# Optimization experiments

Measured on AMD Instinct MI355X. Metric: run time of the kernel, lower is better.

The kernel has to match this reference:

```python
import jax, jax.numpy as jnp
import numpy as np

DIS_NORM = 6.0 * 512 / 1000.0  # 6 * D(z=0) * Nmesh / Boxsize with D(0)=1


def setup_inputs() -> dict:
    key = jax.random.key(0)
    x = jax.random.normal(key, (2, 4, 128, 128, 128), dtype=jnp.float32)
    return {"x": x}


def _lag2eul(x):
    N, C = x.shape[0], x.shape[1]
    D, H, W = x.shape[2], x.shape[3], x.shape[4]
    P = D * H * W
    Cout = C - 3 if C > 3 else 1

    # rm_dis_mean=True: mean displacement, detached
    dis_mean = jax.lax.stop_gradient(jnp.mean(x[:, :3], axis=(2, 3, 4), keepdims=True))

    pos = (x[:, :3] - dis_mean) * DIS_NORM  # (N,3,D,H,W)
    gd = jnp.arange(D, dtype=x.dtype) + 0.5
    gh = jnp.arange(H, dtype=x.dtype) + 0.5
    gw = jnp.arange(W, dtype=x.dtype) + 0.5
    grid = jnp.stack(jnp.meshgrid(gd, gh, gw, indexing='ij'))  # (3,D,H,W)
    pos = (pos + grid[None]).reshape(N, 3, P)

    if C > 3:
        val = x[:, 3:].reshape(N, Cout, P)
    else:
        val = jnp.ones((N, Cout, P), dtype=x.dtype)

    intpos = jnp.floor(pos).astype(jnp.int32)
    # 8 trilinear neighbors: bit b of n -> offset along dim b
    neighbors = (jnp.arange(8, dtype=jnp.int32)[None, :] >> jnp.arange(3, dtype=jnp.int32)[:, None]) & 1  # (3,8)
    tgt = intpos[:, :, :, None] + neighbors[None, :, None, :]  # (N,3,P,8)

    kernel = jnp.prod(1.0 - jnp.abs(pos[:, :, :, None] - tgt.astype(x.dtype)), axis=1)  # (N,P,8)
    src = val[:, :, :, None] * kernel[:, None, :, :]  # (N,Cout,P,8)

    # periodic=False: mask out-of-bounds deposits
    bounds = jnp.array([D, H, W], dtype=jnp.int32)[None, :, None, None]
    mask = jnp.all((tgt >= 0) & (tgt < bounds), axis=1)  # (N,P,8)
    ind = (tgt[:, 0] * H + tgt[:, 1]) * W + tgt[:, 2]  # (N,P,8)
    ind = jnp.clip(ind, 0, P - 1)
    src = jnp.where(mask[:, None, :, :], src, jnp.zeros((), dtype=x.dtype))

    def scatter_one(ind_n, src_n):
        mesh = jnp.zeros((Cout, P), dtype=src_n.dtype)
        return mesh.at[:, ind_n.reshape(-1)].add(src_n.reshape(Cout, -1))

    mesh = jax.vmap(scatter_one)(ind, src)  # (N,Cout,P)
    return mesh.reshape(N, Cout, D, H, W)


def reference(x):
    return _lag2eul(x)
```

## Files before the change

kernel.cpp:

```cpp
#include <hip/hip_runtime.h>

#define NBATCH 2
#define NDIM   128
#define NP     (128 * 128 * 128)
#define DIS_NORM 3.072f

#define TS   16
#define LO   5
#define HI   6
#define WIN  (TS + LO + HI)
#define WIN2 (WIN * WIN)
#define WINF (WIN * WIN * WIN)
#define TPB  8
#define NTILE (TPB * TPB * TPB)
#define NTHR 512

#define FXSCALE 16777216.0f
#define FXINV   (1.0f / 16777216.0f)

#define QCAP 1280

#define SLAB 19696

#define SUMS_OFF 0
#define SLABS_OFF 1024
#define WS_FLOATS ((size_t)SLABS_OFF + (size_t)NBATCH * NTILE * SLAB)
#define WS_NEEDED_BYTES (WS_FLOATS * sizeof(float))

__device__ __constant__ int BASE27[27] = {
    0,216,792,972,1548,3084,3564,3744,4224,
    4376,4952,6488,6968,8504,12600,13880,14360,15640,
    16040,16220,16700,16852,17332,18612,19012,19164,19564};

__global__ __launch_bounds__(256) void prep_kernel(const float* __restrict__ x,
                                                   float* __restrict__ ws,
                                                   float* __restrict__ out) {
    const int plane = blockIdx.y;
    if (plane < 6) {
        const int n = plane / 3, c = plane % 3;
        const float4* xp = (const float4*)(x + ((size_t)n * 4 + c) * NP);
        float s = 0.0f;
        for (int i = blockIdx.x * 256 + threadIdx.x; i < NP / 4; i += 128 * 256) {
            float4 v = xp[i];
            s += (v.x + v.y) + (v.z + v.w);
        }
        #pragma unroll
        for (int off = 32; off > 0; off >>= 1) s += __shfl_down(s, off, 64);
        __shared__ float wsum[4];
        if ((threadIdx.x & 63) == 0) wsum[threadIdx.x >> 6] = s;
        __syncthreads();
        if (threadIdx.x == 0)
            ws[SUMS_OFF + plane * 128 + blockIdx.x] =
                (wsum[0] + wsum[1]) + (wsum[2] + wsum[3]);
    } else {
        float4* o4 = (float4*)out;
        const float4 z = make_float4(0.f, 0.f, 0.f, 0.f);
        for (int i = blockIdx.x * 256 + threadIdx.x; i < NBATCH * NP / 4; i += 128 * 256)
            o4[i] = z;
    }
}

__device__ __forceinline__ void load_means128(const float* __restrict__ ws, int n,
                                              float& m0, float& m1, float& m2) {
    float s0 = 0.f, s1 = 0.f, s2 = 0.f;
    const float* p0 = ws + SUMS_OFF + (n * 3 + 0) * 128;
    const float* p1 = ws + SUMS_OFF + (n * 3 + 1) * 128;
    const float* p2 = ws + SUMS_OFF + (n * 3 + 2) * 128;
    #pragma unroll 4
    for (int b = 0; b < 128; ++b) { s0 += p0[b]; s1 += p1[b]; s2 += p2[b]; }
    const float inv_np = 1.0f / (float)NP;
    m0 = s0 * inv_np; m1 = s1 * inv_np; m2 = s2 * inv_np;
}

__device__ __forceinline__ void deposit_pair(unsigned long long* __restrict__ winU,
                                             int b, float va, float vb) {
    const int fa = __float2int_rn(va * FXSCALE);
    const int fb = __float2int_rn(vb * FXSCALE);
    const bool odd = (b & 1);
    const long long packed = (((long long)fb) << 32) + (long long)fa;
    const long long hiOnly = ((long long)fa) << 32;
    atomicAdd(&winU[b >> 1], (unsigned long long)(odd ? hiOnly : packed));
    if (odd) atomicAdd(&winU[(b >> 1) + 1], (unsigned long long)(long long)fb);
}

__device__ __forceinline__ void slow_deposit(unsigned long long* __restrict__ winU,
                                             float* __restrict__ sp,
                                             float pd, float ph, float pw, float v,
                                             int od, int oh, int ow) {
    const float fd = floorf(pd), fh = floorf(ph), fw = floorf(pw);
    const int id = (int)fd, ih = (int)fh, iw = (int)fw;
    const float rd = pd - fd, rh = ph - fh, rw = pw - fw;
    const int wd = id - od, wh = ih - oh, ww = iw - ow;
    const float wd2[2] = {1.0f - rd, rd};
    const float wh2[2] = {1.0f - rh, rh};
    const float ww2[2] = {1.0f - rw, rw};
    #pragma unroll
    for (int dd = 0; dd < 2; ++dd) {
        const int td = id + dd, wdc = wd + dd;
        const bool dW = (unsigned)wdc < WIN, dM = (unsigned)td < NDIM;
        if (!dM && !dW) continue;
        #pragma unroll
        for (int hh = 0; hh < 2; ++hh) {
            const int th = ih + hh, whc = wh + hh;
            const bool hW = (unsigned)whc < WIN, hM = (unsigned)th < NDIM;
            const float vdh = v * wd2[dd] * wh2[hh];
            #pragma unroll
            for (int wi = 0; wi < 2; ++wi) {
                const int tw = iw + wi, wwc = ww + wi;
                const bool wW = (unsigned)wwc < WIN, wM = (unsigned)tw < NDIM;
                const float dep = vdh * ww2[wi];
                if (dW && hW && wW) {
                    const int cb = (wdc * WIN + whc) * WIN + wwc;
                    const int fx = __float2int_rn(dep * FXSCALE);
                    const long long cv = (cb & 1)
                        ? (((long long)fx) << 32) : (long long)fx;
                    atomicAdd(&winU[cb >> 1], (unsigned long long)cv);
                } else if (dM && hM && wM) {
                    atomicAdd(sp + ((size_t)td * NDIM + th) * NDIM + tw, dep);
                }
            }
        }
    }
}

__global__ __launch_bounds__(NTHR, 4) void scatter_tile_kernel(
        const float* __restrict__ x, const float* __restrict__ ws,
        float* __restrict__ slabs, float* __restrict__ out) {
    const int blk = blockIdx.x;
    const int n = blk >> 9;
    const int t = blk & (NTILE - 1);
    const int tx = t & 7, ty = (t >> 3) & 7, tz = t >> 6;

    __shared__ ulonglong2 win2[(WINF + 3) / 4 + 1];
    __shared__ int qcount;
    __shared__ unsigned short queue[QCAP];
    unsigned long long* winU = (unsigned long long*)win2;
    {
        float4* z4 = (float4*)win2;
        const float4 z = make_float4(0.f, 0.f, 0.f, 0.f);
        for (int i = threadIdx.x; i < (WINF + 3) / 4 + 1; i += NTHR) z4[i] = z;
        if (threadIdx.x == 0) qcount = 0;
    }
    float m0, m1, m2;
    load_means128(ws, n, m0, m1, m2);
    __syncthreads();

    const int i0 = threadIdx.x * 8;
    const int lw0 = i0 & 15;
    const int lh  = (i0 >> 4) & 15;
    const int ld  = i0 >> 8;
    const int gd = tz * TS + ld, gh = ty * TS + lh, gw0 = tx * TS + lw0;
    const size_t prow = ((size_t)gd * NDIM + gh) * NDIM + gw0;

    const float4* x4 = (const float4*)(x + (size_t)n * 4 * NP);
    const size_t q = prow >> 2;
    const size_t s4 = NP / 4;
    float4 a0 = x4[0 * s4 + q], a1 = x4[0 * s4 + q + 1];
    float4 b0 = x4[1 * s4 + q], b1 = x4[1 * s4 + q + 1];
    float4 c0 = x4[2 * s4 + q], c1 = x4[2 * s4 + q + 1];
    float4 e0 = x4[3 * s4 + q], e1 = x4[3 * s4 + q + 1];
    const float D0[8] = {a0.x, a0.y, a0.z, a0.w, a1.x, a1.y, a1.z, a1.w};
    const float D1[8] = {b0.x, b0.y, b0.z, b0.w, b1.x, b1.y, b1.z, b1.w};
    const float D2[8] = {c0.x, c0.y, c0.z, c0.w, c1.x, c1.y, c1.z, c1.w};
    const float VV[8] = {e0.x, e0.y, e0.z, e0.w, e1.x, e1.y, e1.z, e1.w};

    const int od = tz * TS - LO, oh = ty * TS - LO, ow = tx * TS - LO;
    float* sp = out + (size_t)n * NP;

    #pragma unroll
    for (int k = 0; k < 8; ++k) {
        const float pd = (D0[k] - m0) * DIS_NORM + (float)gd + 0.5f;
        const float ph = (D1[k] - m1) * DIS_NORM + (float)gh + 0.5f;
        const float pw = (D2[k] - m2) * DIS_NORM + (float)(gw0 + k) + 0.5f;
        const float v = VV[k];

        const float fd = floorf(pd), fh = floorf(ph), fw = floorf(pw);
        const int id = (int)fd, ih = (int)fh, iw = (int)fw;
        const float rd = pd - fd, rh = ph - fh, rw = pw - fw;

        const int wd = id - od, wh = ih - oh, ww = iw - ow;
        if ((unsigned)wd <= WIN - 2 && (unsigned)wh <= WIN - 2 &&
            (unsigned)ww <= WIN - 2) {
            const int b00 = (wd * WIN + wh) * WIN + ww;
            const float sd0 = v * (1.0f - rd), sd1 = v * rd;
            const float h0 = 1.0f - rh, h1 = rh;
            const float q0 = 1.0f - rw, q1 = rw;
            deposit_pair(winU, b00,              sd0 * h0 * q0, sd0 * h0 * q1);
            deposit_pair(winU, b00 + WIN,        sd0 * h1 * q0, sd0 * h1 * q1);
            deposit_pair(winU, b00 + WIN2,       sd1 * h0 * q0, sd1 * h0 * q1);
            deposit_pair(winU, b00 + WIN2 + WIN, sd1 * h1 * q0, sd1 * h1 * q1);
        } else {
            const int qi = atomicAdd(&qcount, 1);
            if (qi < QCAP) {
                queue[qi] = (unsigned short)(i0 + k);
            } else {
                slow_deposit(winU, sp, pd, ph, pw, v, od, oh, ow);
            }
        }
    }

    __syncthreads();

    {
        const int nq = min(qcount, QCAP);
        const float* xb = x + (size_t)n * 4 * NP;
        for (int qi = threadIdx.x; qi < nq; qi += NTHR) {
            const int p = queue[qi];
            const int lw = p & 15, lhq = (p >> 4) & 15, ldq = p >> 8;
            const int gdq = tz * TS + ldq, ghq = ty * TS + lhq, gwq = tx * TS + lw;
            const size_t pr = ((size_t)gdq * NDIM + ghq) * NDIM + gwq;
            const float pd = (xb[pr] - m0) * DIS_NORM + (float)gdq + 0.5f;
            const float ph = (xb[(size_t)NP + pr] - m1) * DIS_NORM + (float)ghq + 0.5f;
            const float pw = (xb[2 * (size_t)NP + pr] - m2) * DIS_NORM + (float)gwq + 0.5f;
            const float v = xb[3 * (size_t)NP + pr];
            slow_deposit(winU, sp, pd, ph, pw, v, od, oh, ow);
        }
    }
    __syncthreads();

    {
        const int NU = (WINF + 1) / 2;
        for (int i = threadIdx.x; i < NU; i += NTHR) {
            const unsigned long long u = winU[i];
            const int lo = (int)(unsigned)(u & 0xffffffffull);
            const int hi = (int)(u >> 32) + (lo < 0 ? 1 : 0);
            float2 f;
            f.x = (float)lo * FXINV;
            f.y = (float)hi * FXINV;
            ((float2*)winU)[i] = f;
        }
    }
    __syncthreads();
    const float* winF = (const float*)winU;

    const int EXTY[3] = {6, 16, 5};
    const int nbase = n << 9;
    for (int r = threadIdx.x; r < WIN2; r += NTHR) {
        const int lz = r / WIN;
        const int ly = r - lz * WIN;
        int mz, pz;
        if (lz < LO) { mz = -1; pz = lz; }
        else if (lz < LO + TS) { mz = 0; pz = lz - LO; }
        else { mz = 1; pz = lz - LO - TS; }
        int my, py;
        if (ly < LO) { my = -1; py = ly; }
        else if (ly < LO + TS) { my = 0; py = ly - LO; }
        else { my = 1; py = ly - LO - TS; }
        const int dtz = tz + mz, dty = ty + my;
        if ((unsigned)dtz >= TPB || (unsigned)dty >= TPB) continue;

        const int jz = 1 - mz, jy = 1 - my;
        const int ey = EXTY[jy];
        const int rowoff = pz * ey + py;
        const int pobase = jz * 9 + jy * 3;
        const float* src = winF + r * WIN;
        const int slabRow = nbase + (dtz * 8 + dty) * 8;

        if (tx > 0) {
            float* d = slabs + (size_t)(slabRow + tx - 1) * SLAB
                     + BASE27[pobase + 2] + rowoff * 5;
            #pragma unroll
            for (int k = 0; k < 5; ++k) d[k] = src[k];
        }
        {
            float* d = slabs + (size_t)(slabRow + tx) * SLAB
                     + BASE27[pobase + 1] + rowoff * 16;
            #pragma unroll
            for (int k = 0; k < 4; ++k) {
                float4 v;
                v.x = src[5 + 4 * k]; v.y = src[6 + 4 * k];
                v.z = src[7 + 4 * k]; v.w = src[8 + 4 * k];
                ((float4*)d)[k] = v;
            }
        }
        if (tx < TPB - 1) {
            float* d = slabs + (size_t)(slabRow + tx + 1) * SLAB
                     + BASE27[pobase + 0] + rowoff * 6;
            #pragma unroll
            for (int k = 0; k < 6; ++k) d[k] = src[21 + k];
        }
    }
}

__global__ __launch_bounds__(NTHR) void gather_tile_kernel(const float* __restrict__ slabs,
                                                           float* __restrict__ out) {
    const int blk = blockIdx.x;
    const int n = blk >> 9;
    const int t = blk & (NTILE - 1);
    const int tx = t & 7, ty = (t >> 3) & 7, tz = t >> 6;

    const float* __restrict__ slab = slabs + (size_t)blk * SLAB;
    float* __restrict__ ob = out + (size_t)n * NP;

    for (int i = threadIdx.x; i < TS * TS * TS; i += NTHR) {
        const int x = i & 15, y = (i >> 4) & 15, z = i >> 8;

        int zt2 = 0, zp2 = 0, ze2 = 0; bool z2 = false;
        if (z < 6)        { if (tz > 0)       { zt2 = 0;  zp2 = z;      ze2 = 6; z2 = true; } }
        else if (z >= 11) { if (tz < TPB - 1) { zt2 = 18; zp2 = z - 11; ze2 = 5; z2 = true; } }
        int yt2 = 0, yp2 = 0, ye2 = 0; bool y2 = false;
        if (y < 6)        { if (ty > 0)       { yt2 = 0;  yp2 = y;      ye2 = 6; y2 = true; } }
        else if (y >= 11) { if (ty < TPB - 1) { yt2 = 6;  yp2 = y - 11; ye2 = 5; y2 = true; } }
        int xt2 = 0, xp2 = 0, xe2 = 0; bool x2 = false;
        if (x < 6)        { if (tx > 0)       { xt2 = 0;  xp2 = x;      xe2 = 6; x2 = true; } }
        else if (x >= 11) { if (tx < TPB - 1) { xt2 = 2;  xp2 = x - 11; xe2 = 5; x2 = true; } }

        float s = slab[BASE27[13] + (z * 16 + y) * 16 + x];
        if (x2) s += slab[BASE27[9 + 3 + xt2] + (z * 16 + y) * xe2 + xp2];
        if (y2) {
            s += slab[BASE27[9 + yt2 + 1] + (z * ye2 + yp2) * 16 + x];
            if (x2) s += slab[BASE27[9 + yt2 + xt2] + (z * ye2 + yp2) * xe2 + xp2];
        }
        if (z2) {
            s += slab[BASE27[zt2 + 3 + 1] + (zp2 * 16 + y) * 16 + x];
            if (x2) s += slab[BASE27[zt2 + 3 + xt2] + (zp2 * 16 + y) * xe2 + xp2];
            if (y2) {
                s += slab[BASE27[zt2 + yt2 + 1] + (zp2 * ye2 + yp2) * 16 + x];
                if (x2) s += slab[BASE27[zt2 + yt2 + xt2] + (zp2 * ye2 + yp2) * xe2 + xp2];
            }
        }

        const size_t g = (((size_t)(tz * TS + z) * NDIM) + ty * TS + y) * NDIM
                       + tx * TS + x;
        ob[g] += s;
    }
}

__global__ __launch_bounds__(256) void scatter_direct_kernel(const float* __restrict__ x,
                                                             const float* __restrict__ ws,
                                                             float* __restrict__ out) {
    const int lin = blockIdx.x * 256 + threadIdx.x;
    const int n = lin >> 21;
    const int p = lin & (NP - 1);

    float m0, m1, m2;
    load_means128(ws, n, m0, m1, m2);

    const size_t base = (size_t)n * 4 * NP;
    const float d0 = x[base + 0 * (size_t)NP + p];
    const float d1 = x[base + 1 * (size_t)NP + p];
    const float d2 = x[base + 2 * (size_t)NP + p];
    const float v  = x[base + 3 * (size_t)NP + p];

    const int w = p & 127, h = (p >> 7) & 127, d = p >> 14;
    const float pd = (d0 - m0) * DIS_NORM + (float)d + 0.5f;
    const float ph = (d1 - m1) * DIS_NORM + (float)h + 0.5f;
    const float pw = (d2 - m2) * DIS_NORM + (float)w + 0.5f;
    const float fd = floorf(pd), fh = floorf(ph), fw = floorf(pw);
    const int id = (int)fd, ih = (int)fh, iw = (int)fw;
    const float rd = pd - fd, rh = ph - fh, rw = pw - fw;
    const float wd[2] = {1.0f - rd, rd}, wh[2] = {1.0f - rh, rh}, ww[2] = {1.0f - rw, rw};
    float* o = out + (size_t)n * NP;
    #pragma unroll
    for (int dd = 0; dd < 2; ++dd) {
        const int td = id + dd;
        if ((unsigned)td >= (unsigned)NDIM) continue;
        #pragma unroll
        for (int hh = 0; hh < 2; ++hh) {
            const int th = ih + hh;
            if ((unsigned)th >= (unsigned)NDIM) continue;
            const float vdh = v * wd[dd] * wh[hh];
            const int rowbase = (td * NDIM + th) * NDIM;
            #pragma unroll
            for (int wi = 0; wi < 2; ++wi) {
                const int tw = iw + wi;
                if ((unsigned)tw >= (unsigned)NDIM) continue;
                atomicAdd(o + rowbase + tw, vdh * ww[wi]);
            }
        }
    }
}

extern "C" void kernel_launch(void* const* d_in, const int* in_sizes, int n_in,
                              void* d_out, int out_size, void* d_ws, size_t ws_size,
                              hipStream_t stream) {
    const float* x = (const float*)d_in[0];
    float* out = (float*)d_out;
    float* ws = (float*)d_ws;
    float* slabs = ws + SLABS_OFF;

    dim3 pgrid(128, 7);

    if (ws_size >= WS_NEEDED_BYTES) {
        prep_kernel<<<pgrid, 256, 0, stream>>>(x, ws, out);
        scatter_tile_kernel<<<dim3(NBATCH * NTILE), NTHR, 0, stream>>>(x, ws, slabs, out);
        gather_tile_kernel<<<dim3(NBATCH * NTILE), NTHR, 0, stream>>>(slabs, out);
    } else {
        prep_kernel<<<pgrid, 256, 0, stream>>>(x, ws, out);
        scatter_direct_kernel<<<dim3(NBATCH * NP / 256), 256, 0, stream>>>(x, ws, out);
    }
}
```

Before: 198.6 us.

## Shrink tile halo, use fixed-point global spill atomics, compute means per block

After: 236.8 us. 19.2% more time.

```diff
diff --git a/kernel.cpp b/kernel.cpp
--- a/kernel.cpp
+++ b/kernel.cpp
@@ -6,8 +6,8 @@
 #define DIS_NORM 3.072f
 
 #define TS   16
-#define LO   5
-#define HI   6
+#define LO   3
+#define HI   4
 #define WIN  (TS + LO + HI)
 #define WIN2 (WIN * WIN)
 #define WINF (WIN * WIN * WIN)
@@ -18,9 +18,9 @@
 #define FXSCALE 16777216.0f
 #define FXINV   (1.0f / 16777216.0f)
 
-#define QCAP 1280
-
-#define SLAB 19696
+#define QCAP 1024
+
+#define SLAB 12168
 
 #define SUMS_OFF 0
 #define SLABS_OFF 1024
@@ -28,9 +28,9 @@
 #define WS_NEEDED_BYTES (WS_FLOATS * sizeof(float))
 
 __device__ __constant__ int BASE27[27] = {
-    0,216,792,972,1548,3084,3564,3744,4224,
-    4376,4952,6488,6968,8504,12600,13880,14360,15640,
-    16040,16220,16700,16852,17332,18612,19012,19164,19564};
+    0,64,320,368,624,1648,1840,1888,2080,
+    2116,2372,3396,3588,4612,8708,9476,9668,10436,
+    10580,10628,10820,10856,11048,11816,11960,11996,12140};
 
 __global__ __launch_bounds__(256) void prep_kernel(const float* __restrict__ x,
                                                    float* __restrict__ ws,
@@ -84,7 +84,7 @@
 }
 
 __device__ __forceinline__ void slow_deposit(unsigned long long* __restrict__ winU,
-                                             float* __restrict__ sp,
+                                             unsigned int* __restrict__ spU,
                                              float pd, float ph, float pw, float v,
                                              int od, int oh, int ow) {
     const float fd = floorf(pd), fh = floorf(ph), fw = floorf(pw);
@@ -109,21 +109,22 @@
                 const int tw = iw + wi, wwc = ww + wi;
                 const bool wW = (unsigned)wwc < WIN, wM = (unsigned)tw < NDIM;
                 const float dep = vdh * ww2[wi];
+                const int fx = __float2int_rn(dep * FXSCALE);
                 if (dW && hW && wW) {
                     const int cb = (wdc * WIN + whc) * WIN + wwc;
-                    const int fx = __float2int_rn(dep * FXSCALE);
                     const long long cv = (cb & 1)
                         ? (((long long)fx) << 32) : (long long)fx;
                     atomicAdd(&winU[cb >> 1], (unsigned long long)cv);
                 } else if (dM && hM && wM) {
-                    atomicAdd(sp + ((size_t)td * NDIM + th) * NDIM + tw, dep);
+                    atomicAdd(spU + ((size_t)td * NDIM + th) * NDIM + tw,
+                              (unsigned int)fx);
                 }
             }
         }
     }
 }
 
-__global__ __launch_bounds__(NTHR, 4) void scatter_tile_kernel(
+__global__ __launch_bounds__(NTHR, 6) void scatter_tile_kernel(
         const float* __restrict__ x, const float* __restrict__ ws,
         float* __restrict__ slabs, float* __restrict__ out) {
     const int blk = blockIdx.x;
@@ -132,6 +133,7 @@
     const int tx = t & 7, ty = (t >> 3) & 7, tz = t >> 6;
 
     __shared__ ulonglong2 win2[(WINF + 3) / 4 + 1];
+    __shared__ float smean[3];
     __shared__ int qcount;
     __shared__ unsigned short queue[QCAP];
     unsigned long long* winU = (unsigned long long*)win2;
@@ -141,9 +143,17 @@
         for (int i = threadIdx.x; i < (WINF + 3) / 4 + 1; i += NTHR) z4[i] = z;
         if (threadIdx.x == 0) qcount = 0;
     }
-    float m0, m1, m2;
-    load_means128(ws, n, m0, m1, m2);
+    if (threadIdx.x < 192) {
+        const int c = threadIdx.x >> 6;
+        const int l = threadIdx.x & 63;
+        const float* p = ws + SUMS_OFF + (n * 3 + c) * 128;
+        float s = p[l] + p[l + 64];
+        #pragma unroll
+        for (int off = 32; off > 0; off >>= 1) s += __shfl_down(s, off, 64);
+        if (l == 0) smean[c] = s * (1.0f / (float)NP);
+    }
     __syncthreads();
+    const float m0 = smean[0], m1 = smean[1], m2 = smean[2];
 
     const int i0 = threadIdx.x * 8;
     const int lw0 = i0 & 15;
@@ -165,7 +175,7 @@
     const float VV[8] = {e0.x, e0.y, e0.z, e0.w, e1.x, e1.y, e1.z, e1.w};
 
     const int od = tz * TS - LO, oh = ty * TS - LO, ow = tx * TS - LO;
-    float* sp = out + (size_t)n * NP;
+    unsigned int* spU = (unsigned int*)(out + (size_t)n * NP);
 
     #pragma unroll
     for (int k = 0; k < 8; ++k) {
@@ -194,7 +204,7 @@
             if (qi < QCAP) {
                 queue[qi] = (unsigned short)(i0 + k);
             } else {
-                slow_deposit(winU, sp, pd, ph, pw, v, od, oh, ow);
+                slow_deposit(winU, spU, pd, ph, pw, v, od, oh, ow);
             }
         }
     }
@@ -213,7 +223,7 @@
             const float ph = (xb[(size_t)NP + pr] - m1) * DIS_NORM + (float)ghq + 0.5f;
             const float pw = (xb[2 * (size_t)NP + pr] - m2) * DIS_NORM + (float)gwq + 0.5f;
             const float v = xb[3 * (size_t)NP + pr];
-            slow_deposit(winU, sp, pd, ph, pw, v, od, oh, ow);
+            slow_deposit(winU, spU, pd, ph, pw, v, od, oh, ow);
         }
     }
     __syncthreads();
@@ -233,7 +243,7 @@
     __syncthreads();
     const float* winF = (const float*)winU;
 
-    const int EXTY[3] = {6, 16, 5};
+    const int EXTY[3] = {4, 16, 3};
     const int nbase = n << 9;
     for (int r = threadIdx.x; r < WIN2; r += NTHR) {
         const int lz = r / WIN;
@@ -258,9 +268,9 @@
 
         if (tx > 0) {
             float* d = slabs + (size_t)(slabRow + tx - 1) * SLAB
-                     + BASE27[pobase + 2] + rowoff * 5;
+                     + BASE27[pobase + 2] + rowoff * 3;
             #pragma unroll
-            for (int k = 0; k < 5; ++k) d[k] = src[k];
+            for (int k = 0; k < 3; ++k) d[k] = src[k];
         }
         {
             float* d = slabs + (size_t)(slabRow + tx) * SLAB
@@ -268,16 +278,17 @@
             #pragma unroll
             for (int k = 0; k < 4; ++k) {
                 float4 v;
-                v.x = src[5 + 4 * k]; v.y = src[6 + 4 * k];
-                v.z = src[7 + 4 * k]; v.w = src[8 + 4 * k];
+                v.x = src[3 + 4 * k]; v.y = src[4 + 4 * k];
+                v.z = src[5 + 4 * k]; v.w = src[6 + 4 * k];
                 ((float4*)d)[k] = v;
             }
         }
         if (tx < TPB - 1) {
             float* d = slabs + (size_t)(slabRow + tx + 1) * SLAB
-                     + BASE27[pobase + 0] + rowoff * 6;
-            #pragma unroll
-            for (int k = 0; k < 6; ++k) d[k] = src[21 + k];
+                     + BASE27[pobase + 0] + rowoff * 4;
+            float4 v;
+            v.x = src[19]; v.y = src[20]; v.z = src[21]; v.w = src[22];
+            *(float4*)d = v;
         }
     }
 }
@@ -291,19 +302,20 @@
 
     const float* __restrict__ slab = slabs + (size_t)blk * SLAB;
     float* __restrict__ ob = out + (size_t)n * NP;
+    const unsigned int* __restrict__ obU = (const unsigned int*)ob;
 
     for (int i = threadIdx.x; i < TS * TS * TS; i += NTHR) {
         const int x = i & 15, y = (i >> 4) & 15, z = i >> 8;
 
         int zt2 = 0, zp2 = 0, ze2 = 0; bool z2 = false;
-        if (z < 6)        { if (tz > 0)       { zt2 = 0;  zp2 = z;      ze2 = 6; z2 = true; } }
-        else if (z >= 11) { if (tz < TPB - 1) { zt2 = 18; zp2 = z - 11; ze2 = 5; z2 = true; } }
+        if (z < 4)        { if (tz > 0)       { zt2 = 0;  zp2 = z;      ze2 = 4; z2 = true; } }
+        else if (z >= 13) { if (tz < TPB - 1) { zt2 = 18; zp2 = z - 13; ze2 = 3; z2 = true; } }
         int yt2 = 0, yp2 = 0, ye2 = 0; bool y2 = false;
-        if (y < 6)        { if (ty > 0)       { yt2 = 0;  yp2 = y;      ye2 = 6; y2 = true; } }
-        else if (y >= 11) { if (ty < TPB - 1) { yt2 = 6;  yp2 = y - 11; ye2 = 5; y2 = true; } }
+        if (y < 4)        { if (ty > 0)       { yt2 = 0;  yp2 = y;      ye2 = 4; y2 = true; } }
+        else if (y >= 13) { if (ty < TPB - 1) { yt2 = 6;  yp2 = y - 13; ye2 = 3; y2 = true; } }
         int xt2 = 0, xp2 = 0, xe2 = 0; bool x2 = false;
-        if (x < 6)        { if (tx > 0)       { xt2 = 0;  xp2 = x;      xe2 = 6; x2 = true; } }
-        else if (x >= 11) { if (tx < TPB - 1) { xt2 = 2;  xp2 = x - 11; xe2 = 5; x2 = true; } }
+        if (x < 4)        { if (tx > 0)       { xt2 = 0;  xp2 = x;      xe2 = 4; x2 = true; } }
+        else if (x >= 13) { if (tx < TPB - 1) { xt2 = 2;  xp2 = x - 13; xe2 = 3; x2 = true; } }
 
         float s = slab[BASE27[13] + (z * 16 + y) * 16 + x];
         if (x2) s += slab[BASE27[9 + 3 + xt2] + (z * 16 + y) * xe2 + xp2];
@@ -322,7 +334,8 @@
 
         const size_t g = (((size_t)(tz * TS + z) * NDIM) + ty * TS + y) * NDIM
                        + tx * TS + x;
-        ob[g] += s;
+        s += (float)(int)obU[g] * FXINV;
+        ob[g] = s;
     }
 }
 
```

## Replace slab staging and gather pass with direct atomic flush of tile windows

Applied to the files above, without the earlier changes.

Result: slower. 211.8 us (+6.6%).

```diff
diff --git a/kernel.cpp b/kernel.cpp
--- a/kernel.cpp
+++ b/kernel.cpp
@@ -20,17 +20,9 @@
 
 #define QCAP 1280
 
-#define SLAB 19696
-
 #define SUMS_OFF 0
-#define SLABS_OFF 1024
-#define WS_FLOATS ((size_t)SLABS_OFF + (size_t)NBATCH * NTILE * SLAB)
+#define WS_FLOATS 1024
 #define WS_NEEDED_BYTES (WS_FLOATS * sizeof(float))
-
-__device__ __constant__ int BASE27[27] = {
-    0,216,792,972,1548,3084,3564,3744,4224,
-    4376,4952,6488,6968,8504,12600,13880,14360,15640,
-    16040,16220,16700,16852,17332,18612,19012,19164,19564};
 
 __global__ __launch_bounds__(256) void prep_kernel(const float* __restrict__ x,
                                                    float* __restrict__ ws,
@@ -125,13 +117,14 @@
 
 __global__ __launch_bounds__(NTHR, 4) void scatter_tile_kernel(
         const float* __restrict__ x, const float* __restrict__ ws,
-        float* __restrict__ slabs, float* __restrict__ out) {
+        float* __restrict__ out) {
     const int blk = blockIdx.x;
     const int n = blk >> 9;
     const int t = blk & (NTILE - 1);
     const int tx = t & 7, ty = (t >> 3) & 7, tz = t >> 6;
 
     __shared__ ulonglong2 win2[(WINF + 3) / 4 + 1];
+    __shared__ float smean[3];
     __shared__ int qcount;
     __shared__ unsigned short queue[QCAP];
     unsigned long long* winU = (unsigned long long*)win2;
@@ -141,9 +134,17 @@
         for (int i = threadIdx.x; i < (WINF + 3) / 4 + 1; i += NTHR) z4[i] = z;
         if (threadIdx.x == 0) qcount = 0;
     }
-    float m0, m1, m2;
-    load_means128(ws, n, m0, m1, m2);
+    if (threadIdx.x < 192) {
+        const int c = threadIdx.x >> 6;
+        const int l = threadIdx.x & 63;
+        const float* p = ws + SUMS_OFF + (n * 3 + c) * 128;
+        float s = p[l] + p[l + 64];
+        #pragma unroll
+        for (int off = 32; off > 0; off >>= 1) s += __shfl_down(s, off, 64);
+        if (l == 0) smean[c] = s * (1.0f / (float)NP);
+    }
     __syncthreads();
+    const float m0 = smean[0], m1 = smean[1], m2 = smean[2];
 
     const int i0 = threadIdx.x * 8;
     const int lw0 = i0 & 15;
@@ -233,96 +234,17 @@
     __syncthreads();
     const float* winF = (const float*)winU;
 
-    const int EXTY[3] = {6, 16, 5};
-    const int nbase = n << 9;
-    for (int r = threadIdx.x; r < WIN2; r += NTHR) {
-        const int lz = r / WIN;
-        const int ly = r - lz * WIN;
-        int mz, pz;
-        if (lz < LO) { mz = -1; pz = lz; }
-        else if (lz < LO + TS) { mz = 0; pz = lz - LO; }
-        else { mz = 1; pz = lz - LO - TS; }
-        int my, py;
-        if (ly < LO) { my = -1; py = ly; }
-        else if (ly < LO + TS) { my = 0; py = ly - LO; }
-        else { my = 1; py = ly - LO - TS; }
-        const int dtz = tz + mz, dty = ty + my;
-        if ((unsigned)dtz >= TPB || (unsigned)dty >= TPB) continue;
-
-        const int jz = 1 - mz, jy = 1 - my;
-        const int ey = EXTY[jy];
-        const int rowoff = pz * ey + py;
-        const int pobase = jz * 9 + jy * 3;
-        const float* src = winF + r * WIN;
-        const int slabRow = nbase + (dtz * 8 + dty) * 8;
-
-        if (tx > 0) {
-            float* d = slabs + (size_t)(slabRow + tx - 1) * SLAB
-                     + BASE27[pobase + 2] + rowoff * 5;
-            #pragma unroll
-            for (int k = 0; k < 5; ++k) d[k] = src[k];
-        }
-        {
-            float* d = slabs + (size_t)(slabRow + tx) * SLAB
-                     + BASE27[pobase + 1] + rowoff * 16;
-            #pragma unroll
-            for (int k = 0; k < 4; ++k) {
-                float4 v;
-                v.x = src[5 + 4 * k]; v.y = src[6 + 4 * k];
-                v.z = src[7 + 4 * k]; v.w = src[8 + 4 * k];
-                ((float4*)d)[k] = v;
-            }
-        }
-        if (tx < TPB - 1) {
-            float* d = slabs + (size_t)(slabRow + tx + 1) * SLAB
-                     + BASE27[pobase + 0] + rowoff * 6;
-            #pragma unroll
-            for (int k = 0; k < 6; ++k) d[k] = src[21 + k];
-        }
-    }
-}
-
-__global__ __launch_bounds__(NTHR) void gather_tile_kernel(const float* __restrict__ slabs,
-                                                           float* __restrict__ out) {
-    const int blk = blockIdx.x;
-    const int n = blk >> 9;
-    const int t = blk & (NTILE - 1);
-    const int tx = t & 7, ty = (t >> 3) & 7, tz = t >> 6;
-
-    const float* __restrict__ slab = slabs + (size_t)blk * SLAB;
-    float* __restrict__ ob = out + (size_t)n * NP;
-
-    for (int i = threadIdx.x; i < TS * TS * TS; i += NTHR) {
-        const int x = i & 15, y = (i >> 4) & 15, z = i >> 8;
-
-        int zt2 = 0, zp2 = 0, ze2 = 0; bool z2 = false;
-        if (z < 6)        { if (tz > 0)       { zt2 = 0;  zp2 = z;      ze2 = 6; z2 = true; } }
-        else if (z >= 11) { if (tz < TPB - 1) { zt2 = 18; zp2 = z - 11; ze2 = 5; z2 = true; } }
-        int yt2 = 0, yp2 = 0, ye2 = 0; bool y2 = false;
-        if (y < 6)        { if (ty > 0)       { yt2 = 0;  yp2 = y;      ye2 = 6; y2 = true; } }
-        else if (y >= 11) { if (ty < TPB - 1) { yt2 = 6;  yp2 = y - 11; ye2 = 5; y2 = true; } }
-        int xt2 = 0, xp2 = 0, xe2 = 0; bool x2 = false;
-        if (x < 6)        { if (tx > 0)       { xt2 = 0;  xp2 = x;      xe2 = 6; x2 = true; } }
-        else if (x >= 11) { if (tx < TPB - 1) { xt2 = 2;  xp2 = x - 11; xe2 = 5; x2 = true; } }
-
-        float s = slab[BASE27[13] + (z * 16 + y) * 16 + x];
-        if (x2) s += slab[BASE27[9 + 3 + xt2] + (z * 16 + y) * xe2 + xp2];
-        if (y2) {
-            s += slab[BASE27[9 + yt2 + 1] + (z * ye2 + yp2) * 16 + x];
-            if (x2) s += slab[BASE27[9 + yt2 + xt2] + (z * ye2 + yp2) * xe2 + xp2];
-        }
-        if (z2) {
-            s += slab[BASE27[zt2 + 3 + 1] + (zp2 * 16 + y) * 16 + x];
-            if (x2) s += slab[BASE27[zt2 + 3 + xt2] + (zp2 * 16 + y) * xe2 + xp2];
-            if (y2) {
-                s += slab[BASE27[zt2 + yt2 + 1] + (zp2 * ye2 + yp2) * 16 + x];
-                if (x2) s += slab[BASE27[zt2 + yt2 + xt2] + (zp2 * ye2 + yp2) * xe2 + xp2];
-            }
-        }
-
-        const size_t g = (((size_t)(tz * TS + z) * NDIM) + ty * TS + y) * NDIM
-                       + tx * TS + x;
-        ob[g] += s;
+    for (int c = threadIdx.x; c < WINF; c += NTHR) {
+        const int lz = c / WIN2;
+        const int rem = c - lz * WIN2;
+        const int ly = rem / WIN;
+        const int lx = rem - ly * WIN;
+        const int gz = od + lz, gy = oh + ly, gx = ow + lx;
+        const float val = winF[c];
+        if (((unsigned)gz < NDIM) & ((unsigned)gy < NDIM) &
+            ((unsigned)gx < NDIM) & (val != 0.0f)) {
+            atomicAdd(sp + ((size_t)gz * NDIM + gy) * NDIM + gx, val);
+        }
     }
 }
 
@@ -377,14 +299,12 @@
     const float* x = (const float*)d_in[0];
     float* out = (float*)d_out;
     float* ws = (float*)d_ws;
-    float* slabs = ws + SLABS_OFF;
 
     dim3 pgrid(128, 7);
 
     if (ws_size >= WS_NEEDED_BYTES) {
         prep_kernel<<<pgrid, 256, 0, stream>>>(x, ws, out);
-        scatter_tile_kernel<<<dim3(NBATCH * NTILE), NTHR, 0, stream>>>(x, ws, slabs, out);
-        gather_tile_kernel<<<dim3(NBATCH * NTILE), NTHR, 0, stream>>>(slabs, out);
+        scatter_tile_kernel<<<dim3(NBATCH * NTILE), NTHR, 0, stream>>>(x, ws, out);
     } else {
         prep_kernel<<<pgrid, 256, 0, stream>>>(x, ws, out);
         scatter_direct_kernel<<<dim3(NBATCH * NP / 256), 256, 0, stream>>>(x, ws, out);
```
